# Kernel optimization log

Measured on AMD Instinct MI355X. Metric: run time of the kernel, lower is better.

The kernel has to match this reference:

```python
import jax, jax.numpy as jnp
import numpy as np

BIT, ROW, COL = 4, 8, 8
Y_ROW, Z_COL, K = 128, 128, 256  # inter_dimension = 256, K8 = 32
K8 = K // 8
BATCH, SEQ = 8, 2048


def _unpack_bits(packed, n_bits):
    """Unpack uint8 along last axis, big-endian (MSB first), matching np.packbits."""
    shifts = jnp.arange(7, -1, -1, dtype=jnp.uint8)
    bits = (packed[..., None] >> shifts) & jnp.uint8(1)  # [..., k8, 8]
    return bits.reshape(*packed.shape[:-1], -1)[..., :n_bits]


def setup_inputs() -> dict:
    rng = np.random.default_rng(0)
    # Generate underlying binary tensors so Y_sum / Z_sum are consistent with packed bits.
    Yb = rng.integers(0, 2, size=(BIT, ROW, COL, Y_ROW, K), dtype=np.uint8)
    Zb = rng.integers(0, 2, size=(BIT, ROW, COL, K, Z_COL), dtype=np.uint8)
    Y_packed = np.packbits(Yb, axis=-1)                                # [BIT,ROW,COL,Y_ROW,K8]
    Z_packed = np.packbits(Zb.transpose(0, 1, 2, 4, 3), axis=-1)        # [BIT,ROW,COL,Z_COL,K8]
    Y_sum = Yb.sum(axis=-1, keepdims=True).astype(np.int32)             # [BIT,ROW,COL,Y_ROW,1]
    Z_sum = Zb.sum(axis=-2, keepdims=True).astype(np.int32)             # [BIT,ROW,COL,1,Z_COL]

    key = jax.random.key(0)
    k1, k2, k3, k4, k5, k6 = jax.random.split(key, 6)
    X = jax.random.normal(k1, (BATCH, SEQ, COL * Z_COL), dtype=jnp.float32)
    a = jax.random.normal(k2, (BIT, 1, 1, 1, 1), dtype=jnp.float32) * 0.1
    b = jax.random.normal(k3, (BIT, 1, 1, 1, 1), dtype=jnp.float32) * 0.1
    c = jax.random.normal(k4, (BIT, 1, 1, 1, 1), dtype=jnp.float32) * 0.1
    d = jax.random.normal(k5, (1, 1, 1, 1), dtype=jnp.float32) * 0.1
    bias = jax.random.normal(k6, (ROW * Y_ROW,), dtype=jnp.float32) * 0.1
    return {
        "X": X,
        "Y_packed": jnp.asarray(Y_packed),
        "Z_packed": jnp.asarray(Z_packed),
        "Y_sum": jnp.asarray(Y_sum),
        "Z_sum": jnp.asarray(Z_sum),
        "a": a, "b": b, "c": c, "d": d, "bias": bias,
    }


def reference(X, Y_packed, Z_packed, Y_sum, Z_sum, a, b, c, d, bias):
    dtype = X.dtype
    # Unpack bits (fallback path of _matmul_via_unpack) and do binary matmul.
    Y = _unpack_bits(Y_packed, K).astype(dtype)        # [BIT,ROW,COL,Y_ROW,K]
    Zt = _unpack_bits(Z_packed, K).astype(dtype)       # [BIT,ROW,COL,Z_COL,K]
    W_core = jnp.einsum('brcyk,brczk->brcyz', Y, Zt)   # [BIT,ROW,COL,Y_ROW,Z_COL]
    # Affine recombination over bit planes.
    W = a * W_core + b * Y_sum.astype(dtype) + c * Z_sum.astype(dtype)
    W = W.sum(axis=0) + d                               # [ROW,COL,Y_ROW,Z_COL]
    W = W.transpose(0, 2, 1, 3).reshape(ROW * Y_ROW, COL * Z_COL)
    return X @ W.T + bias
```

## Files before the change

kernel.cpp:

```cpp
#include <hip/hip_runtime.h>
#include <hip/hip_bf16.h>
#include <stdint.h>

typedef unsigned int u32;
typedef unsigned short u16;
typedef __attribute__((ext_vector_type(8))) short short8;
typedef __attribute__((ext_vector_type(4))) float floatx4;

#define N_DIM 1024
#define K_DIM 1024
#define M_DIM 16384
#define EPW  68

__device__ __forceinline__ u32 pack4(uint4 v) {
    return (v.x & 0xffu) | ((v.y & 0xffu) << 8) | ((v.z & 0xffu) << 16) | (v.w << 24);
}

__device__ __forceinline__ u16 bf16rne(float f) {
    u32 u = __float_as_uint(f);
    return (u16)((u + 0x7fffu + ((u >> 16) & 1u)) >> 16);
}

__device__ __forceinline__ void load16_lds(const void* g, void* l) {
    __builtin_amdgcn_global_load_lds(
        (const __attribute__((address_space(1))) void*)g,
        (__attribute__((address_space(3))) void*)l, 16, 0, 0);
}

__global__ __launch_bounds__(256) void prep(
        const u32* __restrict__ yp, const u32* __restrict__ zp,
        const int* __restrict__ ysum, const int* __restrict__ zsum,
        const float* __restrict__ pa, const float* __restrict__ pb,
        const float* __restrict__ pc, const float* __restrict__ pd,
        __hip_bfloat16* __restrict__ Wb,
        const float4* __restrict__ X, ushort4* __restrict__ Xb) {
    __shared__ u32 sY[4096];
    __shared__ u32 sZ[1024];
    __shared__ int sYs[512];
    __shared__ int sZs[128];

    const int tid = threadIdx.x;

    if (blockIdx.x >= 256) {
        const size_t base = (size_t)(blockIdx.x - 256) * 512;
        const float4 a = X[base + tid];
        const float4 b = X[base + 256 + tid];
        ushort4 oa, ob;
        oa.x = bf16rne(a.x); oa.y = bf16rne(a.y); oa.z = bf16rne(a.z); oa.w = bf16rne(a.w);
        ob.x = bf16rne(b.x); ob.y = bf16rne(b.y); ob.z = bf16rne(b.z); ob.w = bf16rne(b.w);
        Xb[base + tid] = oa;
        Xb[base + 256 + tid] = ob;
        return;
    }

    const int rc = blockIdx.x >> 2;
    const int zq = blockIdx.x & 3;
    const int r = rc >> 3, c = rc & 7;
    const int z0 = zq * 32;

    const uint4 d0 = ((const uint4*)yp)[0], d1 = ((const uint4*)yp)[1];
    const int sdet = __popc(d0.x) + __popc(d0.y) + __popc(d0.z) + __popc(d0.w)
                   + __popc(d1.x) + __popc(d1.y) + __popc(d1.z) + __popc(d1.w);
    const bool widened = (sdet != ysum[0]);

    if (!widened) {
#pragma unroll
        for (int j = 0; j < 4; ++j) {
            const int chunk = tid + j * 256;
            const int f = chunk * 4;
            const int bit = f >> 10, rem = f & 1023;
            const u32 gw = (u32)((bit * 64 + r * 8 + c) * 1024 + rem);
            ((uint4*)sY)[chunk] = *(const uint4*)(yp + gw);
        }
        {
            const int f = tid * 4;
            const int bit = f >> 8;
            const u32 gw = (u32)((bit * 64 + r * 8 + c) * 1024 + z0 * 8 + (f & 255));
            ((uint4*)sZ)[tid] = *(const uint4*)(zp + gw);
        }
    } else {
#pragma unroll
        for (int j = 0; j < 4; ++j) {
            const int chunk = tid + j * 256;
            const int f = chunk * 4;
            const int bit = f >> 10, rem = f & 1023;
            const u32 gw = (u32)((bit * 64 + r * 8 + c) * 1024 + rem);
            uint4 o;
            o.x = pack4(((const uint4*)yp)[gw + 0]);
            o.y = pack4(((const uint4*)yp)[gw + 1]);
            o.z = pack4(((const uint4*)yp)[gw + 2]);
            o.w = pack4(((const uint4*)yp)[gw + 3]);
            ((uint4*)sY)[chunk] = o;
        }
        {
            const int f = tid * 4;
            const int bit = f >> 8;
            const u32 gw = (u32)((bit * 64 + r * 8 + c) * 1024 + z0 * 8 + (f & 255));
            uint4 o;
            o.x = pack4(((const uint4*)zp)[gw + 0]);
            o.y = pack4(((const uint4*)zp)[gw + 1]);
            o.z = pack4(((const uint4*)zp)[gw + 2]);
            o.w = pack4(((const uint4*)zp)[gw + 3]);
            ((uint4*)sZ)[tid] = o;
        }
    }
    for (int j = tid; j < 512; j += 256) {
        const int bit = j >> 7, y = j & 127;
        sYs[j] = ysum[((bit * 8 + r) * 8 + c) * 128 + y];
    }
    if (tid < 128) {
        const int bit = tid >> 5, zl = tid & 31;
        sZs[tid] = zsum[((bit * 8 + r) * 8 + c) * 128 + z0 + zl];
    }
    __syncthreads();

    float av[4], bv[4], cv[4];
#pragma unroll
    for (int bit = 0; bit < 4; ++bit) { av[bit] = pa[bit]; bv[bit] = pb[bit]; cv[bit] = pc[bit]; }
    const float dv = pd[0];

    const int y = tid & 127;
    const int zh = tid >> 7;

    u32 yw[4][8];
    float base = dv;
#pragma unroll
    for (int bit = 0; bit < 4; ++bit) {
        const uint4 q0 = ((const uint4*)sY)[bit * 256 + y * 2];
        const uint4 q1 = ((const uint4*)sY)[bit * 256 + y * 2 + 1];
        yw[bit][0] = q0.x; yw[bit][1] = q0.y; yw[bit][2] = q0.z; yw[bit][3] = q0.w;
        yw[bit][4] = q1.x; yw[bit][5] = q1.y; yw[bit][6] = q1.z; yw[bit][7] = q1.w;
        base += bv[bit] * (float)sYs[bit * 128 + y];
    }

    const int m = r * 128 + y;
#pragma unroll
    for (int zl2 = 0; zl2 < 16; ++zl2) {
        const int zl = zh * 16 + zl2;
        float wv = base;
#pragma unroll
        for (int bit = 0; bit < 4; ++bit) {
            const uint4 zw0 = ((const uint4*)sZ)[bit * 64 + zl * 2];
            const uint4 zw1 = ((const uint4*)sZ)[bit * 64 + zl * 2 + 1];
            int p = 0;
            p += __popc(yw[bit][0] & zw0.x);
            p += __popc(yw[bit][1] & zw0.y);
            p += __popc(yw[bit][2] & zw0.z);
            p += __popc(yw[bit][3] & zw0.w);
            p += __popc(yw[bit][4] & zw1.x);
            p += __popc(yw[bit][5] & zw1.y);
            p += __popc(yw[bit][6] & zw1.z);
            p += __popc(yw[bit][7] & zw1.w);
            wv += av[bit] * (float)p + cv[bit] * (float)sZs[bit * 32 + zl];
        }
        const int k = c * 128 + z0 + zl;
        Wb[(size_t)m * K_DIM + k] = __float2bfloat16(wv);
    }
}

__device__ __forceinline__ void stage32(const u16* __restrict__ Xb,
        const u16* __restrict__ Wb, int m0, int n0, int kt, char* slot,
        int w, int lane, int srow, int csrc) {
#pragma unroll
    for (int j = 0; j < 4; ++j) {
        const int slab = w * 4 + j;
        const int row = slab * 16 + srow;
        load16_lds(Xb + (size_t)(m0 + row) * K_DIM + kt * 32 + csrc * 8,
                   slot + slab * 1024 + lane * 16);
    }
#pragma unroll
    for (int j = 0; j < 2; ++j) {
        const int slab = w * 2 + j;
        const int row = slab * 16 + srow;
        load16_lds(Wb + (size_t)(n0 + row) * K_DIM + kt * 32 + csrc * 8,
                   slot + 16384 + slab * 1024 + lane * 16);
    }
}

template<bool DO_STAGE, int VM>
__device__ __forceinline__ void tile32(const char* __restrict__ slot,
        char* stslot, int ktg, floatx4 (&acc)[8][4],
        const u16* __restrict__ Xb, const u16* __restrict__ Wb,
        int m0, int n0, int w, int lane, int srow, int csrc,
        int wr, int wc, int fm, int cx) {
    const char* As = slot;
    const char* Bs = slot + 16384;
    short8 a[8], b[4];

#pragma unroll
    for (int mi = 0; mi < 8; ++mi)
        a[mi] = *(const short8*)(As + (wr * 128 + mi * 16 + fm) * 64 + cx);
#pragma unroll
    for (int ni = 0; ni < 4; ++ni)
        b[ni] = *(const short8*)(Bs + (wc * 64 + ni * 16 + fm) * 64 + cx);
    __builtin_amdgcn_s_barrier();
    asm volatile("s_waitcnt lgkmcnt(0)" ::: "memory");
    __builtin_amdgcn_s_setprio(1);
#pragma unroll
    for (int mi = 0; mi < 8; ++mi) {
        acc[mi][0] = __builtin_amdgcn_mfma_f32_16x16x32_bf16(a[mi], b[0], acc[mi][0], 0, 0, 0);
        acc[mi][1] = __builtin_amdgcn_mfma_f32_16x16x32_bf16(a[mi], b[1], acc[mi][1], 0, 0, 0);
    }
    __builtin_amdgcn_s_setprio(0);
    __builtin_amdgcn_s_barrier();

    if (DO_STAGE) stage32(Xb, Wb, m0, n0, ktg, stslot, w, lane, srow, csrc);
    if (VM == 6)      asm volatile("s_waitcnt vmcnt(6)" ::: "memory");
    else              asm volatile("s_waitcnt vmcnt(0)" ::: "memory");
    __builtin_amdgcn_s_barrier();
    __builtin_amdgcn_s_setprio(1);
#pragma unroll
    for (int mi = 0; mi < 8; ++mi) {
        acc[mi][2] = __builtin_amdgcn_mfma_f32_16x16x32_bf16(a[mi], b[2], acc[mi][2], 0, 0, 0);
        acc[mi][3] = __builtin_amdgcn_mfma_f32_16x16x32_bf16(a[mi], b[3], acc[mi][3], 0, 0, 0);
    }
    __builtin_amdgcn_s_setprio(0);
    __builtin_amdgcn_s_barrier();
}

__global__ __launch_bounds__(256, 2) void gemm_bias(
        const u16* __restrict__ Xb, const u16* __restrict__ Wb,
        const float* __restrict__ bias, float* __restrict__ out) {
    __shared__ char lds[49152];

    const int tid = threadIdx.x;
    const int lane = tid & 63;
    const int w = tid >> 6;
    const int wr = w >> 1;
    const int wc = w & 1;
    const int m0 = blockIdx.x * 256;
    const int n0 = blockIdx.y * 128;

    const int srow = lane >> 2;
    const int csrc = (lane & 3) ^ ((lane >> 3) & 3);
    const int fm = lane & 15, fq = lane >> 4;
    const int cx = (fq ^ ((fm >> 1) & 3)) * 16;

    char* slot0 = lds;
    char* slot1 = lds + 24576;

    floatx4 acc[8][4] = {};

    stage32(Xb, Wb, m0, n0, 0, slot0, w, lane, srow, csrc);
    stage32(Xb, Wb, m0, n0, 1, slot1, w, lane, srow, csrc);
    __syncthreads();

    for (int it = 0; it < 15; ++it) {
        tile32<true, 6>(slot0, slot0, 2 * it + 2, acc, Xb, Wb, m0, n0,
                        w, lane, srow, csrc, wr, wc, fm, cx);
        tile32<true, 6>(slot1, slot1, 2 * it + 3, acc, Xb, Wb, m0, n0,
                        w, lane, srow, csrc, wr, wc, fm, cx);
    }
    tile32<false, 0>(slot0, slot0, 0, acc, Xb, Wb, m0, n0,
                     w, lane, srow, csrc, wr, wc, fm, cx);
    tile32<false, 0>(slot1, slot1, 0, acc, Xb, Wb, m0, n0,
                     w, lane, srow, csrc, wr, wc, fm, cx);

    float bias_r[4];
#pragma unroll
    for (int ni = 0; ni < 4; ++ni)
        bias_r[ni] = bias[n0 + wc * 64 + ni * 16 + fm];

    __syncthreads();
    float* ep = (float*)lds + w * (16 * EPW);
    const int gm0 = m0 + wr * 128;
    const int gn0 = n0 + wc * 64;

#pragma unroll
    for (int mi = 0; mi < 8; ++mi) {
#pragma unroll
        for (int ni = 0; ni < 4; ++ni)
#pragma unroll
            for (int reg = 0; reg < 4; ++reg)
                ep[(fq * 4 + reg) * EPW + ni * 16 + fm] = acc[mi][ni][reg] + bias_r[ni];
#pragma unroll
        for (int t = 0; t < 4; ++t) {
            const int lr = t * 4 + fq;
            const float4 v = *(const float4*)(ep + lr * EPW + fm * 4);
            *(float4*)(out + (size_t)(gm0 + mi * 16 + lr) * N_DIM + gn0 + fm * 4) = v;
        }
    }
}

extern "C" void kernel_launch(void* const* d_in, const int* in_sizes, int n_in,
                              void* d_out, int out_size, void* d_ws, size_t ws_size,
                              hipStream_t stream) {
    const float* X   = (const float*)d_in[0];
    const u32*   Yp  = (const u32*)d_in[1];
    const u32*   Zp  = (const u32*)d_in[2];
    const int*   Ys  = (const int*)d_in[3];
    const int*   Zs  = (const int*)d_in[4];
    const float* pa  = (const float*)d_in[5];
    const float* pb  = (const float*)d_in[6];
    const float* pc  = (const float*)d_in[7];
    const float* pd  = (const float*)d_in[8];
    const float* bias = (const float*)d_in[9];
    float* out = (float*)d_out;

    char* ws = (char*)d_ws;
    __hip_bfloat16* Wb = (__hip_bfloat16*)ws;
    u16*            Xb = (u16*)(ws + (2u << 20));

    prep<<<8448, 256, 0, stream>>>(Yp, Zp, Ys, Zs, pa, pb, pc, pd, Wb,
                                   (const float4*)X, (ushort4*)Xb);
    gemm_bias<<<dim3(64, 8), 256, 0, stream>>>(Xb, (const u16*)Wb, bias, out);
}
```

Baseline: 169.6 us.

## Fuse X fp32-to-bf16 conversion into GEMM A-tile staging

Removes the separate conversion pass that wrote a bf16 copy of X to workspace. The GEMM now loads fp32 X into registers, converts it to bf16 and writes it into swizzled LDS after the second MFMA half, while B still uses direct global-to-LDS loads. This saves a kernel phase and the intermediate write/read, but each n-block now re-reads fp32 X (twice the bytes) and register pressure and the synchronization pattern change.

```diff
diff --git a/kernel.cpp b/kernel.cpp
--- a/kernel.cpp
+++ b/kernel.cpp
@@ -27,32 +27,18 @@
         (__attribute__((address_space(3))) void*)l, 16, 0, 0);
 }
 
-__global__ __launch_bounds__(256) void prep(
+__global__ __launch_bounds__(256) void build_w(
         const u32* __restrict__ yp, const u32* __restrict__ zp,
         const int* __restrict__ ysum, const int* __restrict__ zsum,
         const float* __restrict__ pa, const float* __restrict__ pb,
         const float* __restrict__ pc, const float* __restrict__ pd,
-        __hip_bfloat16* __restrict__ Wb,
-        const float4* __restrict__ X, ushort4* __restrict__ Xb) {
+        __hip_bfloat16* __restrict__ Wb) {
     __shared__ u32 sY[4096];
     __shared__ u32 sZ[1024];
     __shared__ int sYs[512];
     __shared__ int sZs[128];
 
     const int tid = threadIdx.x;
-
-    if (blockIdx.x >= 256) {
-        const size_t base = (size_t)(blockIdx.x - 256) * 512;
-        const float4 a = X[base + tid];
-        const float4 b = X[base + 256 + tid];
-        ushort4 oa, ob;
-        oa.x = bf16rne(a.x); oa.y = bf16rne(a.y); oa.z = bf16rne(a.z); oa.w = bf16rne(a.w);
-        ob.x = bf16rne(b.x); ob.y = bf16rne(b.y); ob.z = bf16rne(b.z); ob.w = bf16rne(b.w);
-        Xb[base + tid] = oa;
-        Xb[base + 256 + tid] = ob;
-        return;
-    }
-
     const int rc = blockIdx.x >> 2;
     const int zq = blockIdx.x & 3;
     const int r = rc >> 3, c = rc & 7;
@@ -158,16 +144,8 @@
     }
 }
 
-__device__ __forceinline__ void stage32(const u16* __restrict__ Xb,
-        const u16* __restrict__ Wb, int m0, int n0, int kt, char* slot,
-        int w, int lane, int srow, int csrc) {
-#pragma unroll
-    for (int j = 0; j < 4; ++j) {
-        const int slab = w * 4 + j;
-        const int row = slab * 16 + srow;
-        load16_lds(Xb + (size_t)(m0 + row) * K_DIM + kt * 32 + csrc * 8,
-                   slot + slab * 1024 + lane * 16);
-    }
+__device__ __forceinline__ void stage_b32(const u16* __restrict__ Wb,
+        int n0, int kt, char* slot, int w, int lane, int srow, int csrc) {
 #pragma unroll
     for (int j = 0; j < 2; ++j) {
         const int slab = w * 2 + j;
@@ -177,11 +155,38 @@
     }
 }
 
-template<bool DO_STAGE, int VM>
+__device__ __forceinline__ void load_a32(const float* __restrict__ X,
+        int m0, int kt, int tid, float4 (&ar)[4][2]) {
+#pragma unroll
+    for (int j = 0; j < 4; ++j) {
+        const int row = j * 64 + (tid >> 2);
+        const float* p = X + (size_t)(m0 + row) * K_DIM + kt * 32 + (tid & 3) * 8;
+        ar[j][0] = *(const float4*)p;
+        ar[j][1] = *(const float4*)(p + 4);
+    }
+}
+
+__device__ __forceinline__ void cvt_write_a32(char* slot, int tid,
+        const float4 (&ar)[4][2]) {
+    const int ck = tid & 3;
+#pragma unroll
+    for (int j = 0; j < 4; ++j) {
+        const int row = j * 64 + (tid >> 2);
+        short8 v;
+        v[0] = (short)bf16rne(ar[j][0].x); v[1] = (short)bf16rne(ar[j][0].y);
+        v[2] = (short)bf16rne(ar[j][0].z); v[3] = (short)bf16rne(ar[j][0].w);
+        v[4] = (short)bf16rne(ar[j][1].x); v[5] = (short)bf16rne(ar[j][1].y);
+        v[6] = (short)bf16rne(ar[j][1].z); v[7] = (short)bf16rne(ar[j][1].w);
+        *(short8*)(slot + ((row >> 4) << 10) + ((row & 15) << 6)
+                        + ((ck ^ ((row >> 1) & 3)) << 4)) = v;
+    }
+}
+
+template<bool DO_STAGE>
 __device__ __forceinline__ void tile32(const char* __restrict__ slot,
         char* stslot, int ktg, floatx4 (&acc)[8][4],
-        const u16* __restrict__ Xb, const u16* __restrict__ Wb,
-        int m0, int n0, int w, int lane, int srow, int csrc,
+        const float* __restrict__ X, const u16* __restrict__ Wb,
+        int m0, int n0, int tid, int w, int lane, int srow, int csrc,
         int wr, int wc, int fm, int cx) {
     const char* As = slot;
     const char* Bs = slot + 16384;
@@ -204,10 +209,11 @@
     __builtin_amdgcn_s_setprio(0);
     __builtin_amdgcn_s_barrier();
 
-    if (DO_STAGE) stage32(Xb, Wb, m0, n0, ktg, stslot, w, lane, srow, csrc);
-    if (VM == 6)      asm volatile("s_waitcnt vmcnt(6)" ::: "memory");
-    else              asm volatile("s_waitcnt vmcnt(0)" ::: "memory");
-    __builtin_amdgcn_s_barrier();
+    float4 ar[4][2];
+    if (DO_STAGE) {
+        load_a32(X, m0, ktg, tid, ar);
+        stage_b32(Wb, n0, ktg, stslot, w, lane, srow, csrc);
+    }
     __builtin_amdgcn_s_setprio(1);
 #pragma unroll
     for (int mi = 0; mi < 8; ++mi) {
@@ -215,11 +221,17 @@
         acc[mi][3] = __builtin_amdgcn_mfma_f32_16x16x32_bf16(a[mi], b[3], acc[mi][3], 0, 0, 0);
     }
     __builtin_amdgcn_s_setprio(0);
+    if (DO_STAGE) {
+        asm volatile("s_waitcnt vmcnt(2)" ::: "memory");
+        cvt_write_a32(stslot, tid, ar);
+    } else {
+        asm volatile("s_waitcnt vmcnt(0)" ::: "memory");
+    }
     __builtin_amdgcn_s_barrier();
 }
 
 __global__ __launch_bounds__(256, 2) void gemm_bias(
-        const u16* __restrict__ Xb, const u16* __restrict__ Wb,
+        const float* __restrict__ X, const u16* __restrict__ Wb,
         const float* __restrict__ bias, float* __restrict__ out) {
     __shared__ char lds[49152];
 
@@ -241,20 +253,29 @@
 
     floatx4 acc[8][4] = {};
 
-    stage32(Xb, Wb, m0, n0, 0, slot0, w, lane, srow, csrc);
-    stage32(Xb, Wb, m0, n0, 1, slot1, w, lane, srow, csrc);
+    {
+        float4 ar[4][2];
+        load_a32(X, m0, 0, tid, ar);
+        stage_b32(Wb, n0, 0, slot0, w, lane, srow, csrc);
+        stage_b32(Wb, n0, 1, slot1, w, lane, srow, csrc);
+        asm volatile("s_waitcnt vmcnt(4)" ::: "memory");
+        cvt_write_a32(slot0, tid, ar);
+        load_a32(X, m0, 1, tid, ar);
+        asm volatile("s_waitcnt vmcnt(0)" ::: "memory");
+        cvt_write_a32(slot1, tid, ar);
+    }
     __syncthreads();
 
     for (int it = 0; it < 15; ++it) {
-        tile32<true, 6>(slot0, slot0, 2 * it + 2, acc, Xb, Wb, m0, n0,
-                        w, lane, srow, csrc, wr, wc, fm, cx);
-        tile32<true, 6>(slot1, slot1, 2 * it + 3, acc, Xb, Wb, m0, n0,
-                        w, lane, srow, csrc, wr, wc, fm, cx);
-    }
-    tile32<false, 0>(slot0, slot0, 0, acc, Xb, Wb, m0, n0,
-                     w, lane, srow, csrc, wr, wc, fm, cx);
-    tile32<false, 0>(slot1, slot1, 0, acc, Xb, Wb, m0, n0,
-                     w, lane, srow, csrc, wr, wc, fm, cx);
+        tile32<true>(slot0, slot0, 2 * it + 2, acc, X, Wb, m0, n0,
+                     tid, w, lane, srow, csrc, wr, wc, fm, cx);
+        tile32<true>(slot1, slot1, 2 * it + 3, acc, X, Wb, m0, n0,
+                     tid, w, lane, srow, csrc, wr, wc, fm, cx);
+    }
+    tile32<false>(slot0, slot0, 0, acc, X, Wb, m0, n0,
+                  tid, w, lane, srow, csrc, wr, wc, fm, cx);
+    tile32<false>(slot1, slot1, 0, acc, X, Wb, m0, n0,
+                  tid, w, lane, srow, csrc, wr, wc, fm, cx);
 
     float bias_r[4];
 #pragma unroll
@@ -299,9 +320,7 @@
 
     char* ws = (char*)d_ws;
     __hip_bfloat16* Wb = (__hip_bfloat16*)ws;
-    u16*            Xb = (u16*)(ws + (2u << 20));
-
-    prep<<<8448, 256, 0, stream>>>(Yp, Zp, Ys, Zs, pa, pb, pc, pd, Wb,
-                                   (const float4*)X, (ushort4*)Xb);
-    gemm_bias<<<dim3(64, 8), 256, 0, stream>>>(Xb, (const u16*)Wb, bias, out);
-}
+
+    build_w<<<256, 256, 0, stream>>>(Yp, Zp, Ys, Zs, pa, pb, pc, pd, Wb);
+    gemm_bias<<<dim3(64, 8), 256, 0, stream>>>(X, (const u16*)Wb, bias, out);
+}
```

Measured after the change: 183.9 us. 8.4% more time.

## Load B operand fragments directly from global into registers, bypassing LDS

Applied to the files above, without the earlier changes.

Each wave's W tile fragments now come straight from global memory into a double-buffered register set instead of being staged through LDS. Only the X tile still goes through LDS, which shrinks LDS use from 48KB to 32KB and drops the B LDS reads. The wait and barrier schedule is reworked so the B loads for the next k-tile overlap the second MFMA half. The cost is more VGPRs and uncoalesced-ish 16-byte global loads that are repeated across the waves sharing the same wc.

```diff
diff --git a/kernel.cpp b/kernel.cpp
--- a/kernel.cpp
+++ b/kernel.cpp
@@ -158,9 +158,8 @@
     }
 }
 
-__device__ __forceinline__ void stage32(const u16* __restrict__ Xb,
-        const u16* __restrict__ Wb, int m0, int n0, int kt, char* slot,
-        int w, int lane, int srow, int csrc) {
+__device__ __forceinline__ void stage_a(const u16* __restrict__ Xb,
+        int m0, int kt, char* slot, int w, int lane, int srow, int csrc) {
 #pragma unroll
     for (int j = 0; j < 4; ++j) {
         const int slab = w * 4 + j;
@@ -168,60 +167,57 @@
         load16_lds(Xb + (size_t)(m0 + row) * K_DIM + kt * 32 + csrc * 8,
                    slot + slab * 1024 + lane * 16);
     }
-#pragma unroll
-    for (int j = 0; j < 2; ++j) {
-        const int slab = w * 2 + j;
-        const int row = slab * 16 + srow;
-        load16_lds(Wb + (size_t)(n0 + row) * K_DIM + kt * 32 + csrc * 8,
-                   slot + 16384 + slab * 1024 + lane * 16);
-    }
-}
-
-template<bool DO_STAGE, int VM>
+}
+
+__device__ __forceinline__ void load_b(const u16* __restrict__ Wb,
+        int n0, int kt, int wc, int fm, int fq, short8 (&b)[4]) {
+#pragma unroll
+    for (int ni = 0; ni < 4; ++ni)
+        b[ni] = *(const short8*)(Wb + (size_t)(n0 + wc * 64 + ni * 16 + fm) * K_DIM
+                                 + kt * 32 + fq * 8);
+}
+
+template<bool LOADB, bool STAGEA, int VM>
 __device__ __forceinline__ void tile32(const char* __restrict__ slot,
-        char* stslot, int ktg, floatx4 (&acc)[8][4],
+        char* stslot, int tnext, int tstage, floatx4 (&acc)[8][4],
+        short8 (&bcur)[4], short8 (&bnext)[4],
         const u16* __restrict__ Xb, const u16* __restrict__ Wb,
         int m0, int n0, int w, int lane, int srow, int csrc,
-        int wr, int wc, int fm, int cx) {
-    const char* As = slot;
-    const char* Bs = slot + 16384;
-    short8 a[8], b[4];
+        int wr, int wc, int fm, int fq, int cx) {
+    short8 a[8];
 
 #pragma unroll
     for (int mi = 0; mi < 8; ++mi)
-        a[mi] = *(const short8*)(As + (wr * 128 + mi * 16 + fm) * 64 + cx);
-#pragma unroll
-    for (int ni = 0; ni < 4; ++ni)
-        b[ni] = *(const short8*)(Bs + (wc * 64 + ni * 16 + fm) * 64 + cx);
+        a[mi] = *(const short8*)(slot + (wr * 128 + mi * 16 + fm) * 64 + cx);
     __builtin_amdgcn_s_barrier();
     asm volatile("s_waitcnt lgkmcnt(0)" ::: "memory");
     __builtin_amdgcn_s_setprio(1);
 #pragma unroll
     for (int mi = 0; mi < 8; ++mi) {
-        acc[mi][0] = __builtin_amdgcn_mfma_f32_16x16x32_bf16(a[mi], b[0], acc[mi][0], 0, 0, 0);
-        acc[mi][1] = __builtin_amdgcn_mfma_f32_16x16x32_bf16(a[mi], b[1], acc[mi][1], 0, 0, 0);
+        acc[mi][0] = __builtin_amdgcn_mfma_f32_16x16x32_bf16(a[mi], bcur[0], acc[mi][0], 0, 0, 0);
+        acc[mi][1] = __builtin_amdgcn_mfma_f32_16x16x32_bf16(a[mi], bcur[1], acc[mi][1], 0, 0, 0);
     }
     __builtin_amdgcn_s_setprio(0);
     __builtin_amdgcn_s_barrier();
 
-    if (DO_STAGE) stage32(Xb, Wb, m0, n0, ktg, stslot, w, lane, srow, csrc);
-    if (VM == 6)      asm volatile("s_waitcnt vmcnt(6)" ::: "memory");
-    else              asm volatile("s_waitcnt vmcnt(0)" ::: "memory");
-    __builtin_amdgcn_s_barrier();
+    if (LOADB)  load_b(Wb, n0, tnext, wc, fm, fq, bnext);
+    if (STAGEA) stage_a(Xb, m0, tstage, stslot, w, lane, srow, csrc);
     __builtin_amdgcn_s_setprio(1);
 #pragma unroll
     for (int mi = 0; mi < 8; ++mi) {
-        acc[mi][2] = __builtin_amdgcn_mfma_f32_16x16x32_bf16(a[mi], b[2], acc[mi][2], 0, 0, 0);
-        acc[mi][3] = __builtin_amdgcn_mfma_f32_16x16x32_bf16(a[mi], b[3], acc[mi][3], 0, 0, 0);
+        acc[mi][2] = __builtin_amdgcn_mfma_f32_16x16x32_bf16(a[mi], bcur[2], acc[mi][2], 0, 0, 0);
+        acc[mi][3] = __builtin_amdgcn_mfma_f32_16x16x32_bf16(a[mi], bcur[3], acc[mi][3], 0, 0, 0);
     }
     __builtin_amdgcn_s_setprio(0);
+    if (VM == 4) asm volatile("s_waitcnt vmcnt(4)" ::: "memory");
+    else         asm volatile("s_waitcnt vmcnt(0)" ::: "memory");
     __builtin_amdgcn_s_barrier();
 }
 
 __global__ __launch_bounds__(256, 2) void gemm_bias(
         const u16* __restrict__ Xb, const u16* __restrict__ Wb,
         const float* __restrict__ bias, float* __restrict__ out) {
-    __shared__ char lds[49152];
+    __shared__ char lds[32768];
 
     const int tid = threadIdx.x;
     const int lane = tid & 63;
@@ -237,24 +233,26 @@
     const int cx = (fq ^ ((fm >> 1) & 3)) * 16;
 
     char* slot0 = lds;
-    char* slot1 = lds + 24576;
+    char* slot1 = lds + 16384;
 
     floatx4 acc[8][4] = {};
-
-    stage32(Xb, Wb, m0, n0, 0, slot0, w, lane, srow, csrc);
-    stage32(Xb, Wb, m0, n0, 1, slot1, w, lane, srow, csrc);
+    short8 bA[4], bB[4];
+
+    stage_a(Xb, m0, 0, slot0, w, lane, srow, csrc);
+    stage_a(Xb, m0, 1, slot1, w, lane, srow, csrc);
+    load_b(Wb, n0, 0, wc, fm, fq, bA);
     __syncthreads();
 
     for (int it = 0; it < 15; ++it) {
-        tile32<true, 6>(slot0, slot0, 2 * it + 2, acc, Xb, Wb, m0, n0,
-                        w, lane, srow, csrc, wr, wc, fm, cx);
-        tile32<true, 6>(slot1, slot1, 2 * it + 3, acc, Xb, Wb, m0, n0,
-                        w, lane, srow, csrc, wr, wc, fm, cx);
-    }
-    tile32<false, 0>(slot0, slot0, 0, acc, Xb, Wb, m0, n0,
-                     w, lane, srow, csrc, wr, wc, fm, cx);
-    tile32<false, 0>(slot1, slot1, 0, acc, Xb, Wb, m0, n0,
-                     w, lane, srow, csrc, wr, wc, fm, cx);
+        tile32<true, true, 4>(slot0, slot0, 2 * it + 1, 2 * it + 2, acc, bA, bB,
+                              Xb, Wb, m0, n0, w, lane, srow, csrc, wr, wc, fm, fq, cx);
+        tile32<true, true, 4>(slot1, slot1, 2 * it + 2, 2 * it + 3, acc, bB, bA,
+                              Xb, Wb, m0, n0, w, lane, srow, csrc, wr, wc, fm, fq, cx);
+    }
+    tile32<true, false, 0>(slot0, slot0, 31, 0, acc, bA, bB,
+                           Xb, Wb, m0, n0, w, lane, srow, csrc, wr, wc, fm, fq, cx);
+    tile32<false, false, 0>(slot1, slot1, 0, 0, acc, bB, bA,
+                            Xb, Wb, m0, n0, w, lane, srow, csrc, wr, wc, fm, fq, cx);
 
     float bias_r[4];
 #pragma unroll
```

After: 181.9 us. 1.07x slower.
